# Kernel optimization log

Hardware: AMD Instinct MI355X
Metric: run time of the kernel (lower is better)

## Reference

```python
import jax, jax.numpy as jnp
import numpy as np

BATCH = 512
HIDDEN_DIM = 4096
NUM_CODES = 32
CODE_DIM = 64
CODEBOOK_SIZE = 1024


def _lsa_single(cost):
    """Rectangular Hungarian (Jonker-Volgenant shortest augmenting path).
    cost: [n, m] with n <= m. Returns, for each row, the assigned column,
    minimizing total cost (matches scipy.optimize.linear_sum_assignment)."""
    n, m = cost.shape
    u = np.zeros(n + 1)
    v = np.zeros(m + 1)
    p = np.zeros(m + 1, dtype=np.int64)  # p[j]: row matched to col j (1-based); 0 = free
    for i in range(1, n + 1):
        p[0] = i
        j0 = 0
        minv = np.full(m + 1, np.inf)
        way = np.zeros(m + 1, dtype=np.int64)
        used = np.zeros(m + 1, dtype=bool)
        while True:
            used[j0] = True
            i0 = p[j0]
            free = ~used
            free[0] = False
            jfree = np.nonzero(free)[0]
            cur = cost[i0 - 1, jfree - 1] - u[i0] - v[jfree]
            upd = cur < minv[jfree]
            minv[jfree[upd]] = cur[upd]
            way[jfree[upd]] = j0
            k = jfree[np.argmin(minv[jfree])]
            delta = minv[k]
            u[p[used]] += delta
            v[used] -= delta
            minv[free] -= delta
            j0 = k
            if p[j0] == 0:
                break
        while j0 != 0:  # augment along the path
            j1 = way[j0]
            p[j0] = p[j1]
            j0 = j1
    ans = np.empty(n, dtype=np.int64)
    for j in range(1, m + 1):
        if p[j] > 0:
            ans[p[j] - 1] = j - 1
    return ans


def _lsa_batch(costs):
    costs = np.asarray(costs, dtype=np.float64)
    return np.stack([_lsa_single(c) for c in costs]).astype(np.int32)


def setup_inputs() -> dict:
    key = jax.random.key(0)
    ks = jax.random.split(key, 4)
    return {
        "x": jax.random.normal(ks[0], (BATCH, HIDDEN_DIM), jnp.float32),
        "codebook": jax.random.normal(ks[1], (CODEBOOK_SIZE, CODE_DIM), jnp.float32),
        "enc_w": jax.random.normal(ks[2], (NUM_CODES * CODE_DIM, HIDDEN_DIM), jnp.float32) * 0.02,
        "enc_b": jnp.zeros((NUM_CODES * CODE_DIM,), jnp.float32),
        "dec_w": jax.random.normal(ks[3], (HIDDEN_DIM, NUM_CODES * CODE_DIM), jnp.float32) * 0.02,
        "dec_b": jnp.zeros((HIDDEN_DIM,), jnp.float32),
    }


def reference(x, codebook, enc_w, enc_b, dec_w, dec_b):
    bs = x.shape[0]
    # encoder (torch Linear: y = x @ W.T + b)
    e = (x @ enc_w.T + enc_b).reshape(bs, NUM_CODES, CODE_DIM)
    ef = e.reshape(-1, CODE_DIM)  # [bs*num_codes, code_dim]
    # pairwise Euclidean distances to codebook entries [bs*num_codes, codebook_size]
    d2 = (jnp.sum(ef * ef, axis=1, keepdims=True)
          + jnp.sum(codebook * codebook, axis=1)
          - 2.0 * (ef @ codebook.T))
    dist = jnp.sqrt(jnp.maximum(d2, 0.0)).reshape(bs, NUM_CODES, CODEBOOK_SIZE)
    # per-sample Hungarian assignment (original uses scipy on CPU; sqrt is
    # monotone so the optimal assignment is identical)
    indices = jax.pure_callback(
        _lsa_batch,
        jax.ShapeDtypeStruct((bs, NUM_CODES), jnp.int32),
        jax.lax.stop_gradient(dist),
    )
    flat_idx = indices.reshape(-1)  # matches torch's concatenated flat indices
    q = codebook[flat_idx].reshape(bs, NUM_CODES, CODE_DIM)
    # straight-through estimator
    q_st = e + jax.lax.stop_gradient(q - e)
    r = q_st.reshape(bs, NUM_CODES * CODE_DIM) @ dec_w.T + dec_b
    return (r, q, e, flat_idx)
```

## Files before the change

### kernel.cpp

```cpp
#include <hip/hip_runtime.h>
#include <hip/hip_bf16.h>
#include <stdint.h>

#define BATCH 512
#define HID   4096
#define NC    32
#define CD    64
#define CB    1024
#define NCD   2048

typedef unsigned short u16;
typedef unsigned int   u32;
typedef __attribute__((ext_vector_type(8))) short short8;
typedef __attribute__((ext_vector_type(4))) float f32x4;

#define WAVE_SYNC()  asm volatile("s_waitcnt lgkmcnt(0)" ::: "memory")
#define SCHED_FENCE() __builtin_amdgcn_sched_barrier(0)

__device__ inline u16 bf16_rne(float f) {
  u32 u = __builtin_bit_cast(u32, f);
  u32 r = u + 0x7FFFu + ((u >> 16) & 1u);
  return (u16)(r >> 16);
}
__device__ inline float bf16_f32(u16 h) {
  u32 u = ((u32)h) << 16;
  return __builtin_bit_cast(float, u);
}
__device__ inline void split3(float a, u16& h1, u16& h2, u16& h3) {
  h1 = bf16_rne(a);
  float r1 = a - bf16_f32(h1);
  h2 = bf16_rne(r1);
  float r2 = r1 - bf16_f32(h2);
  h3 = bf16_rne(r2);
}
__device__ inline f32x4 mfma16(short8 a, short8 b, f32x4 c) {
  return __builtin_amdgcn_mfma_f32_16x16x32_bf16(a, b, c, 0, 0, 0);
}
__device__ inline void gload_lds16(const u16* g, u16* l) {
  __builtin_amdgcn_global_load_lds(
      (const __attribute__((address_space(1))) u32*)(const void*)g,
      (__attribute__((address_space(3))) u32*)(void*)l, 16, 0, 0);
}

union H8 { u16 h[8]; short8 v; };

template<int K>
__global__ __launch_bounds__(256) void conv_split3(
    const float* __restrict__ src, u16* __restrict__ d1,
    u16* __restrict__ d2, u16* __restrict__ d3) {
  const int t = threadIdx.x;
  const int g = blockIdx.x * 4 + (t >> 6);
  const int l = t & 63;
  const int n  = (g / (K / 32)) * 16 + (l & 15);
  const int k0 = (g % (K / 32)) * 32 + (l >> 4) * 8;
  const float* s = src + (size_t)n * K + k0;
  H8 o1, o2, o3;
#pragma unroll
  for (int i = 0; i < 8; ++i) split3(s[i], o1.h[i], o2.h[i], o3.h[i]);
  size_t off = (size_t)g * 512 + l * 8;
  *(short8*)(d1 + off) = o1.v;
  *(short8*)(d2 + off) = o2.v;
  *(short8*)(d3 + off) = o3.v;
}

template<int K>
__global__ __launch_bounds__(256) void conv_split1(
    const float* __restrict__ src, u16* __restrict__ d1) {
  const int t = threadIdx.x;
  const int g = blockIdx.x * 4 + (t >> 6);
  const int l = t & 63;
  const int n  = (g / (K / 32)) * 16 + (l & 15);
  const int k0 = (g % (K / 32)) * 32 + (l >> 4) * 8;
  const float* s = src + (size_t)n * K + k0;
  H8 o1;
#pragma unroll
  for (int i = 0; i < 8; ++i) o1.h[i] = bf16_rne(s[i]);
  *(short8*)(d1 + (size_t)g * 512 + l * 8) = o1.v;
}

__global__ __launch_bounds__(512) void k1_gemm(
    const float* __restrict__ A,
    const u16* __restrict__ B1, const u16* __restrict__ B2,
    const u16* __restrict__ B3, float* __restrict__ part) {
  __shared__ u16 As[2][3][8][64][8];
  __shared__ u16 Bs[2][3][8][64][8];
  const int t = threadIdx.x;
  const int wid = t >> 6, lane = t & 63;
  const int wrow = wid >> 2, wcol = wid & 3;
  const int bm = blockIdx.x * 128;
  const int bn = blockIdx.y * 128;
  const int kz = blockIdx.z;
  const int kbase = kz * 1024;
  const int arow = t >> 2;
  const int akc  = t & 3;
  const float* aptr = A + (size_t)(bm + arow) * HID + kbase + akc * 8;
  const int arf = arow >> 4;
  const int p_w = (akc << 4) | (arow & 15);
  const int s_w = p_w ^ ((p_w >> 4) & 3);
  const int s_r = lane ^ ((lane >> 4) & 3);
  const size_t nf0 = (size_t)((bn >> 4) + wid);

  f32x4 acc[4][2];
#pragma unroll
  for (int r = 0; r < 4; ++r)
#pragma unroll
    for (int c = 0; c < 2; ++c) acc[r][c] = (f32x4)0.f;

  {
    float va[8];
    *(f32x4*)&va[0] = *(const f32x4*)(aptr);
    *(f32x4*)&va[4] = *(const f32x4*)(aptr + 4);
    size_t gb = (nf0 * 128 + (size_t)(kbase >> 5)) * 512 + lane * 8;
    gload_lds16(B1 + gb, &Bs[0][0][wid][0][0]);
    gload_lds16(B2 + gb, &Bs[0][1][wid][0][0]);
    gload_lds16(B3 + gb, &Bs[0][2][wid][0][0]);
    H8 s1, s2, s3;
#pragma unroll
    for (int i = 0; i < 8; ++i) split3(va[i], s1.h[i], s2.h[i], s3.h[i]);
    *(short8*)&As[0][0][arf][s_w][0] = s1.v;
    *(short8*)&As[0][1][arf][s_w][0] = s2.v;
    *(short8*)&As[0][2][arf][s_w][0] = s3.v;
  }
  __syncthreads();

  for (int ks = 0; ks < 32; ++ks) {
    const int cur = ks & 1, nxt = cur ^ 1;
    float vb[8];
    if (ks < 31) {
      *(f32x4*)&vb[0] = *(const f32x4*)(aptr + (ks + 1) * 32);
      *(f32x4*)&vb[4] = *(const f32x4*)(aptr + (ks + 1) * 32 + 4);
      size_t gb = (nf0 * 128 + (size_t)((kbase >> 5) + ks + 1)) * 512 + lane * 8;
      gload_lds16(B1 + gb, &Bs[nxt][0][wid][0][0]);
      gload_lds16(B2 + gb, &Bs[nxt][1][wid][0][0]);
      gload_lds16(B3 + gb, &Bs[nxt][2][wid][0][0]);
    }
    short8 a0[4], a1[4], a2[4], b0[2], b1[2], b2[2];
#pragma unroll
    for (int r = 0; r < 4; ++r) {
      a0[r] = *(const short8*)&As[cur][0][wrow * 4 + r][s_r][0];
      a1[r] = *(const short8*)&As[cur][1][wrow * 4 + r][s_r][0];
      a2[r] = *(const short8*)&As[cur][2][wrow * 4 + r][s_r][0];
    }
#pragma unroll
    for (int c = 0; c < 2; ++c) {
      b0[c] = *(const short8*)&Bs[cur][0][wcol * 2 + c][lane][0];
      b1[c] = *(const short8*)&Bs[cur][1][wcol * 2 + c][lane][0];
      b2[c] = *(const short8*)&Bs[cur][2][wcol * 2 + c][lane][0];
    }
#pragma unroll
    for (int r = 0; r < 4; ++r)
#pragma unroll
      for (int c = 0; c < 2; ++c) {
        f32x4 d = acc[r][c];
        d = mfma16(a0[r], b0[c], d);
        d = mfma16(a0[r], b1[c], d);
        d = mfma16(a1[r], b0[c], d);
        d = mfma16(a1[r], b1[c], d);
        d = mfma16(a0[r], b2[c], d);
        d = mfma16(a2[r], b0[c], d);
        acc[r][c] = d;
      }
    if (ks < 31) {
      H8 s1, s2, s3;
#pragma unroll
      for (int i = 0; i < 8; ++i) split3(vb[i], s1.h[i], s2.h[i], s3.h[i]);
      *(short8*)&As[nxt][0][arf][s_w][0] = s1.v;
      *(short8*)&As[nxt][1][arf][s_w][0] = s2.v;
      *(short8*)&As[nxt][2][arf][s_w][0] = s3.v;
    }
    __syncthreads();
  }
  float* P = part + (size_t)kz * BATCH * NCD;
#pragma unroll
  for (int r = 0; r < 4; ++r)
#pragma unroll
    for (int c = 0; c < 2; ++c) {
      int row = bm + wrow * 64 + r * 16 + (lane >> 4) * 4;
      int col = bn + wcol * 32 + c * 16 + (lane & 15);
#pragma unroll
      for (int i = 0; i < 4; ++i)
        P[(size_t)(row + i) * NCD + col] = acc[r][c][i];
    }
}

__global__ __launch_bounds__(256) void k_reduce_bias(
    const float* __restrict__ part, const float* __restrict__ bias,
    float* __restrict__ e) {
  size_t o = ((size_t)blockIdx.x * 256 + threadIdx.x) * 4;
  int n = (int)(o & (NCD - 1));
  f32x4 s = *(const f32x4*)(part + o);
  s += *(const f32x4*)(part + (size_t)1 * BATCH * NCD + o);
  s += *(const f32x4*)(part + (size_t)2 * BATCH * NCD + o);
  s += *(const f32x4*)(part + (size_t)3 * BATCH * NCD + o);
  s += *(const f32x4*)(bias + n);
  *(f32x4*)(e + o) = s;
}

__global__ __launch_bounds__(512) void k3_gemm(
    const u16* __restrict__ Ab, const u16* __restrict__ Bb,
    const float* __restrict__ bias, float* __restrict__ C) {
  __shared__ u16 As[4][64][8];
  __shared__ u16 Bs[8][64][8];
  const int t = threadIdx.x;
  const int wid = t >> 6, lane = t & 63;
  const int wrow = wid >> 2, wcol = wid & 3;
  const int bm = blockIdx.x * 64, bn = blockIdx.y * 128;
  f32x4 acc[2][2];
#pragma unroll
  for (int r = 0; r < 2; ++r)
#pragma unroll
    for (int c = 0; c < 2; ++c) acc[r][c] = (f32x4)0.f;

  for (int ks = 0; ks < 64; ++ks) {
    {
      size_t gb = (((size_t)(bn >> 4) + wid) * 64 + ks) * 512 + lane * 8;
      gload_lds16(Bb + gb, &Bs[wid][0][0]);
      if (wid < 4) {
        size_t ga = (((size_t)(bm >> 4) + wid) * 64 + ks) * 512 + lane * 8;
        gload_lds16(Ab + ga, &As[wid][0][0]);
      }
    }
    __syncthreads();
    short8 a[2], b[2];
#pragma unroll
    for (int r = 0; r < 2; ++r) a[r] = *(const short8*)&As[wrow * 2 + r][lane][0];
#pragma unroll
    for (int c = 0; c < 2; ++c) b[c] = *(const short8*)&Bs[wcol * 2 + c][lane][0];
#pragma unroll
    for (int r = 0; r < 2; ++r)
#pragma unroll
      for (int c = 0; c < 2; ++c) acc[r][c] = mfma16(a[r], b[c], acc[r][c]);
    __syncthreads();
  }
#pragma unroll
  for (int r = 0; r < 2; ++r)
#pragma unroll
    for (int c = 0; c < 2; ++c) {
      int row = bm + wrow * 32 + r * 16 + (lane >> 4) * 4;
      int col = bn + wcol * 32 + c * 16 + (lane & 15);
      float bb = bias[col];
#pragma unroll
      for (int i = 0; i < 4; ++i)
        C[(size_t)(row + i) * HID + col] = acc[r][c][i] + bb;
    }
}

__global__ __launch_bounds__(256) void k_cost(
    const float* __restrict__ e_glob, const float* __restrict__ codebook,
    float* __restrict__ cost) {
  __shared__ float es[64][68];
  __shared__ float cs[64][68];
  __shared__ float enorm[64], cnorm[64];
  const int t = threadIdx.x;
  const int r0 = blockIdx.x * 64;
  const int c0 = blockIdx.y * 256;
  const int tx = t & 15, ty = t >> 4;
  {
    int row = t & 63, kq = t >> 6;
    const float* src = e_glob + (size_t)(r0 + row) * 64 + kq * 16;
#pragma unroll
    for (int i = 0; i < 4; ++i) {
      float4 v = *(const float4*)(src + i * 4);
      int kk = kq * 16 + i * 4;
      es[kk + 0][row] = v.x; es[kk + 1][row] = v.y;
      es[kk + 2][row] = v.z; es[kk + 3][row] = v.w;
    }
  }
  __syncthreads();
  if (t < 64) {
    float s = 0.f;
    for (int kk = 0; kk < 64; ++kk) { float x = es[kk][t]; s = fmaf(x, x, s); }
    enorm[t] = s;
  }
  for (int sub = 0; sub < 4; ++sub) {
    __syncthreads();
    {
      int col = t & 63, kq = t >> 6;
      const float* src = codebook + (size_t)(c0 + sub * 64 + col) * 64 + kq * 16;
#pragma unroll
      for (int i = 0; i < 4; ++i) {
        float4 v = *(const float4*)(src + i * 4);
        int kk = kq * 16 + i * 4;
        cs[kk + 0][col] = v.x; cs[kk + 1][col] = v.y;
        cs[kk + 2][col] = v.z; cs[kk + 3][col] = v.w;
      }
    }
    __syncthreads();
    if (t < 64) {
      float s = 0.f;
      for (int kk = 0; kk < 64; ++kk) { float x = cs[kk][t]; s = fmaf(x, x, s); }
      cnorm[t] = s;
    }
    __syncthreads();
    float dot[4][4] = {};
#pragma unroll 8
    for (int kk = 0; kk < 64; ++kk) {
      float4 a4 = *(const float4*)&es[kk][ty * 4];
      float4 b4 = *(const float4*)&cs[kk][tx * 4];
      float a_[4] = {a4.x, a4.y, a4.z, a4.w};
      float b_[4] = {b4.x, b4.y, b4.z, b4.w};
#pragma unroll
      for (int i = 0; i < 4; ++i)
#pragma unroll
        for (int j = 0; j < 4; ++j)
          dot[i][j] = fmaf(a_[i], b_[j], dot[i][j]);
    }
#pragma unroll
    for (int i = 0; i < 4; ++i) {
      int r = ty * 4 + i;
      float en = enorm[r];
      float4 o;
      o.x = sqrtf(fmaxf(en + cnorm[tx * 4 + 0] - 2.f * dot[i][0], 0.f));
      o.y = sqrtf(fmaxf(en + cnorm[tx * 4 + 1] - 2.f * dot[i][1], 0.f));
      o.z = sqrtf(fmaxf(en + cnorm[tx * 4 + 2] - 2.f * dot[i][2], 0.f));
      o.w = sqrtf(fmaxf(en + cnorm[tx * 4 + 3] - 2.f * dot[i][3], 0.f));
      *(float4*)&cost[(size_t)(r0 + r) * CB + c0 + sub * 64 + tx * 4] = o;
    }
  }
}

__global__ __launch_bounds__(64, 1) void k_assign(
    const float* __restrict__ cost_g, const float* __restrict__ codebook,
    float* __restrict__ q_out, float* __restrict__ idx_out) {
  __shared__ int idxl[32];
  const int lane = threadIdx.x;
  const int s = blockIdx.x;
  const float* __restrict__ cost = cost_g + (size_t)s * NC * CB;

  double v_[16], minv_[16];
  u32 wp_[16];
  double u_val = 0.0;
#pragma unroll
  for (int r = 0; r < 16; ++r) { v_[r] = 0.0; wp_[r] = 0; }

  float pf[16];
#pragma unroll
  for (int r = 0; r < 16; ++r) pf[r] = cost[r * 64 + lane];

  for (int i = 1; i <= NC; ++i) {
#pragma unroll
    for (int r = 0; r < 16; ++r) minv_[r] = 1e300;
    u32 col_used = 0;
    unsigned long long rowmask = 0ull;
    int j0 = 0;
    int i0 = i;
    int first = 1;
    for (int guard = 0; guard < 1056; ++guard) {
      rowmask |= (1ull << i0);
      const double ui0 = __shfl(u_val, i0);
      float cc[16];
      if (first) {
#pragma unroll
        for (int r = 0; r < 16; ++r) cc[r] = pf[r];
        if (i < NC) {
#pragma unroll
          for (int r = 0; r < 16; ++r)
            pf[r] = cost[(size_t)i * CB + r * 64 + lane];
        }
        first = 0;
      } else {
        const float* crow = cost + (size_t)(i0 - 1) * CB;
#pragma unroll
        for (int r = 0; r < 16; ++r) cc[r] = crow[r * 64 + lane];
      }
      double bv = 1e301; int bj = 1 << 20;
#pragma unroll
      for (int r = 0; r < 16; ++r) {
        const int j = 1 + lane + r * 64;
        if (!((col_used >> r) & 1u)) {
          double cur = (double)cc[r] - ui0 - v_[r];
          if (cur < minv_[r]) { minv_[r] = cur; wp_[r] = (wp_[r] & 0xFFFF0000u) | (u32)j0; }
          if (minv_[r] < bv) { bv = minv_[r]; bj = j; }
        }
      }
#pragma unroll
      for (int off = 1; off < 64; off <<= 1) {
        double ov = __shfl_xor(bv, off);
        int oj = __shfl_xor(bj, off);
        if (ov < bv || (ov == bv && oj < bj)) { bv = ov; bj = oj; }
      }
      const double delta = bv;
      const int k = bj;
      if ((rowmask >> lane) & 1ull) u_val += delta;
#pragma unroll
      for (int r = 0; r < 16; ++r) {
        const int j = 1 + lane + r * 64;
        if ((col_used >> r) & 1u) v_[r] -= delta;
        else {
          minv_[r] -= delta;
          if (j == k) col_used |= (1u << r);
        }
      }
      const int rk = (k - 1) >> 6, kl = (k - 1) & 63;
      u32 sel = 0;
#pragma unroll
      for (int r = 0; r < 16; ++r) if (r == rk) sel = wp_[r];
      const int pmk = ((u32)__shfl((int)sel, kl)) >> 16;
      j0 = k;
      if (pmk == 0) break;
      i0 = pmk;
    }
    int jj = j0;
    while (jj != 0) {
      const int rj = (jj - 1) >> 6, lj = (jj - 1) & 63;
      u32 wsel = 0;
#pragma unroll
      for (int r = 0; r < 16; ++r) if (r == rj) wsel = wp_[r];
      const int j1 = ((u32)__shfl((int)wsel, lj)) & 0xFFFFu;
      int newpm;
      if (j1 == 0) newpm = i;
      else {
        const int r1 = (j1 - 1) >> 6, l1 = (j1 - 1) & 63;
        u32 psel = 0;
#pragma unroll
        for (int r = 0; r < 16; ++r) if (r == r1) psel = wp_[r];
        newpm = ((u32)__shfl((int)psel, l1)) >> 16;
      }
#pragma unroll
      for (int r = 0; r < 16; ++r)
        if (lane == lj && r == rj) wp_[r] = (wp_[r] & 0xFFFFu) | ((u32)newpm << 16);
      jj = j1;
    }
  }

#pragma unroll
  for (int r = 0; r < 16; ++r) {
    const u32 pm = wp_[r] >> 16;
    if (pm > 0) idxl[pm - 1] = lane + r * 64;
  }
  WAVE_SYNC(); SCHED_FENCE();
  if (lane < NC) idx_out[(size_t)s * NC + lane] = (float)idxl[lane];
#pragma unroll
  for (int p = 0; p < 8; ++p) {
    int vi = p * 64 + lane;
    int r = vi >> 4, c4 = vi & 15;
    int ci = idxl[r];
    float4 qv = *(const float4*)&codebook[(size_t)ci * 64 + c4 * 4];
    *(float4*)&q_out[(size_t)s * NCD + r * 64 + c4 * 4] = qv;
  }
}

extern "C" void kernel_launch(void* const* d_in, const int* in_sizes, int n_in,
                              void* d_out, int out_size, void* d_ws, size_t ws_size,
                              hipStream_t stream) {
  (void)in_sizes; (void)n_in; (void)out_size; (void)ws_size;
  const float* x        = (const float*)d_in[0];
  const float* codebook = (const float*)d_in[1];
  const float* enc_w    = (const float*)d_in[2];
  const float* enc_b    = (const float*)d_in[3];
  const float* dec_w    = (const float*)d_in[4];
  const float* dec_b    = (const float*)d_in[5];

  float* out = (float*)d_out;
  float* r_out   = out;
  float* q_out   = out + 2097152;
  float* e_out   = out + 2097152 + 1048576;
  float* idx_out = out + 2097152 + 2097152;

  char* ws = (char*)d_ws;
  u16* B1 = (u16*)ws;
  u16* B2 = (u16*)(ws + (16u << 20));
  u16* B3 = (u16*)(ws + (32u << 20));
  float* part = (float*)(ws + (48u << 20));
  float* cost_ws = (float*)ws;
  u16* qb  = (u16*)ws;
  u16* dwb = (u16*)(ws + (2u << 20));

  conv_split3<HID><<<4096, 256, 0, stream>>>(enc_w, B1, B2, B3);
  k1_gemm<<<dim3(4, 16, 4), 512, 0, stream>>>(x, B1, B2, B3, part);
  k_reduce_bias<<<1024, 256, 0, stream>>>(part, enc_b, e_out);
  k_cost<<<dim3(16384 / 64, CB / 256), 256, 0, stream>>>(e_out, codebook, cost_ws);
  k_assign<<<BATCH, 64, 0, stream>>>(cost_ws, codebook, q_out, idx_out);
  conv_split1<NCD><<<4096, 256, 0, stream>>>(dec_w, dwb);
  conv_split1<NCD><<<512, 256, 0, stream>>>(q_out, qb);
  k3_gemm<<<dim3(8, 32), 512, 0, stream>>>(qb, dwb, dec_b, r_out);
}
```

Before: 232.2 us.

## Use split-bf16 MFMA for cost matrix, coalesce conversions, remap GEMM blocks per XCD

The distance kernel now computes its dot products with three-way split-bf16 MFMA on 128x128 tiles, where it previously used scalar FP32 FMAs, and it computes norms directly from global memory. The conversion kernels stage their inputs through shared memory so global reads are coalesced rows instead of strided per-lane reads. Both GEMMs remap block indices so neighbouring tiles land on the same XCD for better L2 reuse. The split-bf16 path approximates FP32 accuracy, which could shift near-tie assignments.

```diff
diff --git a/kernel.cpp b/kernel.cpp
--- a/kernel.cpp
+++ b/kernel.cpp
@@ -48,15 +48,24 @@
 __global__ __launch_bounds__(256) void conv_split3(
     const float* __restrict__ src, u16* __restrict__ d1,
     u16* __restrict__ d2, u16* __restrict__ d3) {
+  __shared__ float st[4][16][36];
   const int t = threadIdx.x;
-  const int g = blockIdx.x * 4 + (t >> 6);
-  const int l = t & 63;
-  const int n  = (g / (K / 32)) * 16 + (l & 15);
-  const int k0 = (g % (K / 32)) * 32 + (l >> 4) * 8;
-  const float* s = src + (size_t)n * K + k0;
+  const int wv = t >> 6, l = t & 63;
+  const int g = blockIdx.x * 4 + wv;
+  const int rowbase = (g / (K / 32)) * 16;
+  const int kbase   = (g % (K / 32)) * 32;
+  {
+    const float* s = src + (size_t)(rowbase + (l >> 2)) * K + kbase + (l & 3) * 8;
+    *(f32x4*)&st[wv][l >> 2][(l & 3) * 8]     = *(const f32x4*)s;
+    *(f32x4*)&st[wv][l >> 2][(l & 3) * 8 + 4] = *(const f32x4*)(s + 4);
+  }
+  __syncthreads();
+  float vv[8];
+  *(f32x4*)&vv[0] = *(const f32x4*)&st[wv][l & 15][(l >> 4) * 8];
+  *(f32x4*)&vv[4] = *(const f32x4*)&st[wv][l & 15][(l >> 4) * 8 + 4];
   H8 o1, o2, o3;
 #pragma unroll
-  for (int i = 0; i < 8; ++i) split3(s[i], o1.h[i], o2.h[i], o3.h[i]);
+  for (int i = 0; i < 8; ++i) split3(vv[i], o1.h[i], o2.h[i], o3.h[i]);
   size_t off = (size_t)g * 512 + l * 8;
   *(short8*)(d1 + off) = o1.v;
   *(short8*)(d2 + off) = o2.v;
@@ -66,15 +75,24 @@
 template<int K>
 __global__ __launch_bounds__(256) void conv_split1(
     const float* __restrict__ src, u16* __restrict__ d1) {
+  __shared__ float st[4][16][36];
   const int t = threadIdx.x;
-  const int g = blockIdx.x * 4 + (t >> 6);
-  const int l = t & 63;
-  const int n  = (g / (K / 32)) * 16 + (l & 15);
-  const int k0 = (g % (K / 32)) * 32 + (l >> 4) * 8;
-  const float* s = src + (size_t)n * K + k0;
+  const int wv = t >> 6, l = t & 63;
+  const int g = blockIdx.x * 4 + wv;
+  const int rowbase = (g / (K / 32)) * 16;
+  const int kbase   = (g % (K / 32)) * 32;
+  {
+    const float* s = src + (size_t)(rowbase + (l >> 2)) * K + kbase + (l & 3) * 8;
+    *(f32x4*)&st[wv][l >> 2][(l & 3) * 8]     = *(const f32x4*)s;
+    *(f32x4*)&st[wv][l >> 2][(l & 3) * 8 + 4] = *(const f32x4*)(s + 4);
+  }
+  __syncthreads();
+  float vv[8];
+  *(f32x4*)&vv[0] = *(const f32x4*)&st[wv][l & 15][(l >> 4) * 8];
+  *(f32x4*)&vv[4] = *(const f32x4*)&st[wv][l & 15][(l >> 4) * 8 + 4];
   H8 o1;
 #pragma unroll
-  for (int i = 0; i < 8; ++i) o1.h[i] = bf16_rne(s[i]);
+  for (int i = 0; i < 8; ++i) o1.h[i] = bf16_rne(vv[i]);
   *(short8*)(d1 + (size_t)g * 512 + l * 8) = o1.v;
 }
 
@@ -87,9 +105,12 @@
   const int t = threadIdx.x;
   const int wid = t >> 6, lane = t & 63;
   const int wrow = wid >> 2, wcol = wid & 3;
-  const int bm = blockIdx.x * 128;
-  const int bn = blockIdx.y * 128;
-  const int kz = blockIdx.z;
+  const int d = blockIdx.x + (blockIdx.y << 2) + (blockIdx.z << 6);
+  const int xcd = d & 7, sl = d >> 3;
+  const int panel = (xcd << 3) + (sl >> 2);
+  const int bm = (sl & 3) * 128;
+  const int bn = (panel & 15) * 128;
+  const int kz = panel >> 4;
   const int kbase = kz * 1024;
   const int arow = t >> 2;
   const int akc  = t & 3;
@@ -151,14 +172,14 @@
     for (int r = 0; r < 4; ++r)
 #pragma unroll
       for (int c = 0; c < 2; ++c) {
-        f32x4 d = acc[r][c];
-        d = mfma16(a0[r], b0[c], d);
-        d = mfma16(a0[r], b1[c], d);
-        d = mfma16(a1[r], b0[c], d);
-        d = mfma16(a1[r], b1[c], d);
-        d = mfma16(a0[r], b2[c], d);
-        d = mfma16(a2[r], b0[c], d);
-        acc[r][c] = d;
+        f32x4 dd = acc[r][c];
+        dd = mfma16(a0[r], b0[c], dd);
+        dd = mfma16(a0[r], b1[c], dd);
+        dd = mfma16(a1[r], b0[c], dd);
+        dd = mfma16(a1[r], b1[c], dd);
+        dd = mfma16(a0[r], b2[c], dd);
+        dd = mfma16(a2[r], b0[c], dd);
+        acc[r][c] = dd;
       }
     if (ks < 31) {
       H8 s1, s2, s3;
@@ -204,7 +225,10 @@
   const int t = threadIdx.x;
   const int wid = t >> 6, lane = t & 63;
   const int wrow = wid >> 2, wcol = wid & 3;
-  const int bm = blockIdx.x * 64, bn = blockIdx.y * 128;
+  const int d = blockIdx.x + (blockIdx.y << 3);
+  const int xcd = d & 7, sl = d >> 3;
+  const int bn = ((xcd << 2) + (sl >> 3)) * 128;
+  const int bm = (sl & 7) * 64;
   f32x4 acc[2][2];
 #pragma unroll
   for (int r = 0; r < 2; ++r)
@@ -245,78 +269,105 @@
     }
 }
 
-__global__ __launch_bounds__(256) void k_cost(
-    const float* __restrict__ e_glob, const float* __restrict__ codebook,
+__global__ __launch_bounds__(512) void k_cost(
+    const float* __restrict__ e_glob,
+    const float* __restrict__ codebook,
     float* __restrict__ cost) {
-  __shared__ float es[64][68];
-  __shared__ float cs[64][68];
-  __shared__ float enorm[64], cnorm[64];
+  __shared__ u16 Ea[2][3][8][64][8];
+  __shared__ u16 Cbs[2][3][8][64][8];
+  __shared__ float enorm[128], cnorm[128];
   const int t = threadIdx.x;
-  const int r0 = blockIdx.x * 64;
-  const int c0 = blockIdx.y * 256;
-  const int tx = t & 15, ty = t >> 4;
+  const int wid = t >> 6, lane = t & 63;
+  const int wrow = wid >> 2, wcol = wid & 3;
+  const int r0 = blockIdx.x * 128;
+  const int c0 = blockIdx.y * 128;
+
   {
-    int row = t & 63, kq = t >> 6;
-    const float* src = e_glob + (size_t)(r0 + row) * 64 + kq * 16;
-#pragma unroll
-    for (int i = 0; i < 4; ++i) {
-      float4 v = *(const float4*)(src + i * 4);
-      int kk = kq * 16 + i * 4;
-      es[kk + 0][row] = v.x; es[kk + 1][row] = v.y;
-      es[kk + 2][row] = v.z; es[kk + 3][row] = v.w;
-    }
+    const int fr = lane & 15, kc = lane >> 4;
+    const float* ea = e_glob   + (size_t)(r0 + wid * 16 + fr) * CD + kc * 8;
+    const float* cb = codebook + (size_t)(c0 + wid * 16 + fr) * CD + kc * 8;
+#pragma unroll
+    for (int ks = 0; ks < 2; ++ks) {
+      float va[8], vb[8];
+      *(f32x4*)&va[0] = *(const f32x4*)(ea + ks * 32);
+      *(f32x4*)&va[4] = *(const f32x4*)(ea + ks * 32 + 4);
+      *(f32x4*)&vb[0] = *(const f32x4*)(cb + ks * 32);
+      *(f32x4*)&vb[4] = *(const f32x4*)(cb + ks * 32 + 4);
+      H8 a1, a2, a3, b1, b2, b3;
+#pragma unroll
+      for (int i = 0; i < 8; ++i) {
+        split3(va[i], a1.h[i], a2.h[i], a3.h[i]);
+        split3(vb[i], b1.h[i], b2.h[i], b3.h[i]);
+      }
+      *(short8*)&Ea[ks][0][wid][lane][0] = a1.v;
+      *(short8*)&Ea[ks][1][wid][lane][0] = a2.v;
+      *(short8*)&Ea[ks][2][wid][lane][0] = a3.v;
+      *(short8*)&Cbs[ks][0][wid][lane][0] = b1.v;
+      *(short8*)&Cbs[ks][1][wid][lane][0] = b2.v;
+      *(short8*)&Cbs[ks][2][wid][lane][0] = b3.v;
+    }
+  }
+  if (t < 256) {
+    const int which = t >> 7, idx = t & 127;
+    const float* p = which ? codebook + (size_t)(c0 + idx) * CD
+                           : e_glob   + (size_t)(r0 + idx) * CD;
+    float s = 0.f;
+#pragma unroll
+    for (int k = 0; k < 16; ++k) {
+      f32x4 v = *(const f32x4*)(p + k * 4);
+      s += v.x * v.x + v.y * v.y + v.z * v.z + v.w * v.w;
+    }
+    if (which) cnorm[idx] = s; else enorm[idx] = s;
   }
   __syncthreads();
-  if (t < 64) {
-    float s = 0.f;
-    for (int kk = 0; kk < 64; ++kk) { float x = es[kk][t]; s = fmaf(x, x, s); }
-    enorm[t] = s;
-  }
-  for (int sub = 0; sub < 4; ++sub) {
-    __syncthreads();
-    {
-      int col = t & 63, kq = t >> 6;
-      const float* src = codebook + (size_t)(c0 + sub * 64 + col) * 64 + kq * 16;
+
+  f32x4 acc[4][2];
+#pragma unroll
+  for (int r = 0; r < 4; ++r)
+#pragma unroll
+    for (int c = 0; c < 2; ++c) acc[r][c] = (f32x4)0.f;
+#pragma unroll
+  for (int ks = 0; ks < 2; ++ks) {
+    short8 a0[4], a1[4], a2[4], b0[2], b1[2], b2[2];
+#pragma unroll
+    for (int r = 0; r < 4; ++r) {
+      a0[r] = *(const short8*)&Ea[ks][0][wrow * 4 + r][lane][0];
+      a1[r] = *(const short8*)&Ea[ks][1][wrow * 4 + r][lane][0];
+      a2[r] = *(const short8*)&Ea[ks][2][wrow * 4 + r][lane][0];
+    }
+#pragma unroll
+    for (int c = 0; c < 2; ++c) {
+      b0[c] = *(const short8*)&Cbs[ks][0][wcol * 2 + c][lane][0];
+      b1[c] = *(const short8*)&Cbs[ks][1][wcol * 2 + c][lane][0];
+      b2[c] = *(const short8*)&Cbs[ks][2][wcol * 2 + c][lane][0];
+    }
+#pragma unroll
+    for (int r = 0; r < 4; ++r)
+#pragma unroll
+      for (int c = 0; c < 2; ++c) {
+        f32x4 dd = acc[r][c];
+        dd = mfma16(a0[r], b0[c], dd);
+        dd = mfma16(a0[r], b1[c], dd);
+        dd = mfma16(a1[r], b0[c], dd);
+        dd = mfma16(a1[r], b1[c], dd);
+        dd = mfma16(a0[r], b2[c], dd);
+        dd = mfma16(a2[r], b0[c], dd);
+        acc[r][c] = dd;
+      }
+  }
+#pragma unroll
+  for (int r = 0; r < 4; ++r)
+#pragma unroll
+    for (int c = 0; c < 2; ++c) {
+      const int rl = wrow * 64 + r * 16 + (lane >> 4) * 4;
+      const int cl = wcol * 32 + c * 16 + (lane & 15);
+      const float cn = cnorm[cl];
 #pragma unroll
       for (int i = 0; i < 4; ++i) {
-        float4 v = *(const float4*)(src + i * 4);
-        int kk = kq * 16 + i * 4;
-        cs[kk + 0][col] = v.x; cs[kk + 1][col] = v.y;
-        cs[kk + 2][col] = v.z; cs[kk + 3][col] = v.w;
-      }
-    }
-    __syncthreads();
-    if (t < 64) {
-      float s = 0.f;
-      for (int kk = 0; kk < 64; ++kk) { float x = cs[kk][t]; s = fmaf(x, x, s); }
-      cnorm[t] = s;
-    }
-    __syncthreads();
-    float dot[4][4] = {};
-#pragma unroll 8
-    for (int kk = 0; kk < 64; ++kk) {
-      float4 a4 = *(const float4*)&es[kk][ty * 4];
-      float4 b4 = *(const float4*)&cs[kk][tx * 4];
-      float a_[4] = {a4.x, a4.y, a4.z, a4.w};
-      float b_[4] = {b4.x, b4.y, b4.z, b4.w};
-#pragma unroll
-      for (int i = 0; i < 4; ++i)
-#pragma unroll
-        for (int j = 0; j < 4; ++j)
-          dot[i][j] = fmaf(a_[i], b_[j], dot[i][j]);
-    }
-#pragma unroll
-    for (int i = 0; i < 4; ++i) {
-      int r = ty * 4 + i;
-      float en = enorm[r];
-      float4 o;
-      o.x = sqrtf(fmaxf(en + cnorm[tx * 4 + 0] - 2.f * dot[i][0], 0.f));
-      o.y = sqrtf(fmaxf(en + cnorm[tx * 4 + 1] - 2.f * dot[i][1], 0.f));
-      o.z = sqrtf(fmaxf(en + cnorm[tx * 4 + 2] - 2.f * dot[i][2], 0.f));
-      o.w = sqrtf(fmaxf(en + cnorm[tx * 4 + 3] - 2.f * dot[i][3], 0.f));
-      *(float4*)&cost[(size_t)(r0 + r) * CB + c0 + sub * 64 + tx * 4] = o;
-    }
-  }
+        float d2 = enorm[rl + i] + cn - 2.f * acc[r][c][i];
+        cost[(size_t)(r0 + rl + i) * CB + c0 + cl] = sqrtf(fmaxf(d2, 0.f));
+      }
+    }
 }
 
 __global__ __launch_bounds__(64, 1) void k_assign(
@@ -469,7 +520,7 @@
   conv_split3<HID><<<4096, 256, 0, stream>>>(enc_w, B1, B2, B3);
   k1_gemm<<<dim3(4, 16, 4), 512, 0, stream>>>(x, B1, B2, B3, part);
   k_reduce_bias<<<1024, 256, 0, stream>>>(part, enc_b, e_out);
-  k_cost<<<dim3(16384 / 64, CB / 256), 256, 0, stream>>>(e_out, codebook, cost_ws);
+  k_cost<<<dim3(128, 8), 512, 0, stream>>>(e_out, codebook, cost_ws);
   k_assign<<<BATCH, 64, 0, stream>>>(cost_ws, codebook, q_out, idx_out);
   conv_split1<NCD><<<4096, 256, 0, stream>>>(dec_w, dwb);
   conv_split1<NCD><<<512, 256, 0, stream>>>(q_out, qb);
```

Measured after the change: 221.0 us. 1.05x faster.
